# Optimization experiments

Hardware: AMD Instinct MI355X
Metric: run time of the kernel (lower is better)

## Reference

```python
import jax, jax.numpy as jnp
import numpy as np

NUM_TAGS = 5

def setup_inputs() -> dict:
    key = jax.random.key(0)
    ks = jax.random.split(key, 8)
    B, N, K, Q = 2, 5, 5, 4
    Ls, Lq, D = 128, 128, 768
    inp = {
        'support_token_embedding': jax.random.normal(ks[0], (B * N * K, Ls, D), jnp.float32),
        'query_token_embedding': jax.random.normal(ks[1], (B * N * Q, Lq, D), jnp.float32),
        'support_mask': jnp.ones((B * N * K, Ls), jnp.float32),
        'query_mask': jnp.ones((B * N * Q, Lq), jnp.float32),
        'support_entity_label': jax.random.normal(ks[2], (B * N * K, Ls, NUM_TAGS), jnp.float32),
        'proj_w': jax.random.normal(ks[3], (D, 4 * D), jnp.float32) * 0.02,
        'proj_b': jnp.zeros((D,), jnp.float32),
        'rel_w1': jax.random.normal(ks[4], (D, 4 * D), jnp.float32) * 0.02,
        'rel_b1': jnp.zeros((D,), jnp.float32),
        'rel_w2': jax.random.normal(ks[5], (1, D), jnp.float32) * 0.02,
        'rel_b2': jnp.zeros((1,), jnp.float32),
        'B': B, 'N': N, 'K': K, 'Q': Q,
    }
    return inp

def _fuse(m1, m2):
    return jnp.concatenate([m1, m2, jnp.abs(m1 - m2), m1 * m2], axis=-1)

def reference(support_token_embedding, query_token_embedding, support_mask, query_mask,
              support_entity_label, proj_w, proj_b, rel_w1, rel_b1, rel_w2, rel_b2,
              B, N, K, Q):
    D = support_token_embedding.shape[-1]
    Lq = query_token_embedding.shape[1]

    # ---- cal_bio: per-(sample,shot) tag prototypes, vectorized ----
    labels = jnp.argmax(support_entity_label, axis=-1)                 # [BNK, Ls]
    onehot = jax.nn.one_hot(labels, NUM_TAGS, dtype=jnp.float32)       # [BNK, Ls, T]
    # tag 0 ('O') is additionally gated by the support mask
    masks = jnp.concatenate([onehot[:, :, :1] * support_mask[:, :, None], onehot[:, :, 1:]], axis=2)
    sums = jnp.einsum('blt,bld->btd', masks, support_token_embedding)  # [BNK, T, D]
    cnt = jnp.sum(masks, axis=1)[:, :, None]                           # [BNK, T, 1]
    proto = jnp.where(cnt > 0, sums / jnp.maximum(cnt, 1.0), 0.0)      # [BNK, T, D]
    proto = proto.reshape(B * N, K, NUM_TAGS, D).mean(axis=1)          # mean over K shots
    proto = proto.reshape(B, N, NUM_TAGS, D)                           # support_BIO

    # ---- expand to all (query, class) pairs: batch = B*N*Q*N ----
    BQ = B * N * Q * N
    support = jnp.broadcast_to(proto[:, None], (B, N * Q, N, NUM_TAGS, D)).reshape(BQ, NUM_TAGS, D)
    query = jnp.broadcast_to(query_token_embedding.reshape(B, N * Q, 1, Lq, D),
                             (B, N * Q, N, Lq, D)).reshape(BQ, Lq, D)
    qmask = jnp.broadcast_to(query_mask.reshape(B, N * Q, 1, Lq),
                             (B, N * Q, N, Lq)).reshape(BQ, Lq, 1)
    smask = jnp.ones((BQ, NUM_TAGS, 1), jnp.float32)

    # ---- CoAttention with additive mask bias + post-softmax mask multiply ----
    att = jnp.einsum('bsd,bqd->bsq', support, query) + smask * jnp.swapaxes(qmask, 1, 2) * 100.0
    support_ = jnp.einsum('bsq,bqd->bsd', jax.nn.softmax(att, axis=2), query) * smask
    query_ = jnp.einsum('bqs,bsd->bqd', jax.nn.softmax(jnp.swapaxes(att, 1, 2), axis=2), support) * qmask

    # ---- fuse + proj + relu ----
    es = jax.nn.relu(_fuse(support, support_) @ proj_w.T + proj_b)     # [BQ, T, D]
    eq = jax.nn.relu(_fuse(query, query_) @ proj_w.T + proj_b)        # [BQ, Lq, D]

    # ---- local aggregation: masked max + mean pooling ----
    eq_agg = jnp.concatenate([jnp.max(eq, axis=1), jnp.sum(eq, axis=1) / jnp.sum(qmask, axis=1)], axis=1)
    es_agg = jnp.concatenate([jnp.max(es, axis=1), jnp.sum(es, axis=1) / jnp.sum(smask, axis=1)], axis=1)

    # ---- relation MLP ----
    cat_seq = jnp.concatenate([eq_agg, es_agg], axis=1)                # [BQ, 4D]
    h = jax.nn.relu(cat_seq @ rel_w1.T + rel_b1)
    logits = h @ rel_w2.T + rel_b2                                     # [BQ, 1]
    return logits.reshape(B * N * Q, N)
```

## Files before the change

### kernel.cpp

```cpp
#include <hip/hip_runtime.h>

typedef unsigned short u16;
typedef __attribute__((ext_vector_type(8))) short short8;
typedef __attribute__((ext_vector_type(4))) float f32x4;

#define B_   2
#define N_   5
#define K_   5
#define Q_   4
#define T_   5
#define D_   768
#define L_   128
#define BN_  (B_*N_)
#define BNK_ (B_*N_*K_)
#define BQ_  (B_*N_*Q_*N_)
#define K4_  (4*D_)
#define KFQ  1536
#define AROWS 144

#define QEMB_N  (40*128*768)
#define PROJW_N (768*3072)

__device__ __forceinline__ float bf2f(u16 u) {
    return __uint_as_float(((unsigned)u) << 16);
}
__device__ __forceinline__ u16 f2bf(float f) {
    unsigned u = __float_as_uint(f);
    return (u16)((u + 0x7fffu + ((u >> 16) & 1u)) >> 16);
}
__device__ __forceinline__ void gl_lds16(const u16* g, u16* l) {
    __builtin_amdgcn_global_load_lds(
        (const __attribute__((address_space(1))) unsigned int*)g,
        (__attribute__((address_space(3))) unsigned int*)l, 16, 0, 0);
}

__global__ void k_convert3(const float* __restrict__ q, const float* __restrict__ pw,
                           const float* __restrict__ rw, u16* __restrict__ qo,
                           u16* __restrict__ po, u16* __restrict__ ro) {
    const long n1 = QEMB_N / 4, n2 = PROJW_N / 4;
    const long total = n1 + 2 * n2;
    for (long i = (long)blockIdx.x * 256 + threadIdx.x; i < total; i += (long)gridDim.x * 256) {
        const float* src; u16* dst; long k;
        if (i < n1)            { src = q;  dst = qo; k = i; }
        else if (i < n1 + n2)  { src = pw; dst = po; k = i - n1; }
        else                   { src = rw; dst = ro; k = i - n1 - n2; }
        float4 v = ((const float4*)src)[k];
        u16 o[4] = {f2bf(v.x), f2bf(v.y), f2bf(v.z), f2bf(v.w)};
        *(uint2*)(dst + k * 4) = *(const uint2*)o;
    }
}

__global__ void k_proto_shot(const float* __restrict__ label, const float* __restrict__ smask,
                             const float* __restrict__ semb, float* __restrict__ proto_shot) {
    int bnk = blockIdx.x;
    __shared__ int   s_tag[L_];
    __shared__ float s_w[L_];
    __shared__ float s_cnt[T_];
    int tid = threadIdx.x;
    if (tid < L_) {
        const float* lp = label + ((long)bnk * L_ + tid) * T_;
        float best = lp[0]; int bi = 0;
        #pragma unroll
        for (int t = 1; t < T_; ++t) { float v = lp[t]; if (v > best) { best = v; bi = t; } }
        s_tag[tid] = bi;
        s_w[tid]   = (bi == 0) ? smask[(long)bnk * L_ + tid] : 1.0f;
    }
    __syncthreads();
    if (tid < T_) {
        float c = 0.f;
        for (int l = 0; l < L_; ++l) if (s_tag[l] == tid) c += s_w[l];
        s_cnt[tid] = c;
    }
    __syncthreads();
    float acc[3][T_] = {};
    for (int l = 0; l < L_; ++l) {
        float w = s_w[l]; int tg = s_tag[l];
        const float* ep = semb + ((long)bnk * L_ + l) * D_;
        #pragma unroll
        for (int s = 0; s < 3; ++s) {
            float e = ep[tid + s * 256] * w;
            #pragma unroll
            for (int t = 0; t < T_; ++t) acc[s][t] += (tg == t) ? e : 0.0f;
        }
    }
    #pragma unroll
    for (int s = 0; s < 3; ++s) {
        int d = tid + s * 256;
        #pragma unroll
        for (int t = 0; t < T_; ++t) {
            float c = s_cnt[t];
            float v = (c > 0.f) ? acc[s][t] / fmaxf(c, 1.f) : 0.f;
            proto_shot[(bnk * T_ + t) * D_ + d] = v;
        }
    }
}

__global__ void k_proto_mean(const float* __restrict__ proto_shot,
                             float* __restrict__ proto_f32, u16* __restrict__ proto_bf) {
    int idx = blockIdx.x * 256 + threadIdx.x;
    if (idx >= BN_ * T_ * D_) return;
    int bn = idx / (T_ * D_);
    int rem = idx - bn * (T_ * D_);
    float s = 0.f;
    #pragma unroll
    for (int k = 0; k < K_; ++k) s += proto_shot[(bn * K_ + k) * (T_ * D_) + rem];
    s *= (1.f / K_);
    proto_f32[idx] = s;
    proto_bf[idx]  = f2bf(s);
}

__global__ void k_attn(const float* __restrict__ qemb, const float* __restrict__ qmask_g,
                       const float* __restrict__ proto_f32,
                       u16* __restrict__ qf, u16* __restrict__ sup_ws,
                       float* __restrict__ p2m_ws, float* __restrict__ qssum_ws) {
    int x = blockIdx.x;
    int xcd = x & 7, slot = x >> 3;
    int g = (slot / 5) * 8 + xcd;
    int n2 = slot % 5;
    int bq = g * 5 + n2;
    int q_idx = g;
    int bn = (bq / (N_ * Q_ * N_)) * N_ + (bq % N_);
    __shared__ float s_proto[T_ * D_];
    __shared__ float s_att[T_][L_];
    __shared__ float s_ps[T_][L_];
    __shared__ float s_p2[L_][8];
    __shared__ float s_qm[L_];
    int tid = threadIdx.x;
    int w = tid >> 6, lane = tid & 63;
    for (int i = tid; i < T_ * D_; i += 256) s_proto[i] = proto_f32[bn * T_ * D_ + i];
    if (tid < L_) s_qm[tid] = qmask_g[(long)q_idx * L_ + tid];
    __syncthreads();
    for (int p = tid; p < T_ * L_; p += 256) {
        int t = p >> 7, q = p & (L_ - 1);
        const float* pp = s_proto + t * D_;
        const float4* qp = (const float4*)(qemb + ((size_t)q_idx * L_ + q) * D_);
        float acc = 0.f;
        #pragma unroll 4
        for (int d = 0; d < D_ / 4; ++d) {
            float4 v = qp[d];
            acc += v.x * pp[4 * d] + v.y * pp[4 * d + 1] + v.z * pp[4 * d + 2] + v.w * pp[4 * d + 3];
        }
        s_att[t][q] = acc + 100.f * s_qm[q];
    }
    __syncthreads();
    if (tid < T_) {
        int t = tid; float m = -1e30f;
        for (int q = 0; q < L_; ++q) m = fmaxf(m, s_att[t][q]);
        float ss = 0.f;
        for (int q = 0; q < L_; ++q) { float e = __expf(s_att[t][q] - m); s_ps[t][q] = e; ss += e; }
        float inv = 1.f / ss;
        for (int q = 0; q < L_; ++q) s_ps[t][q] *= inv;
    } else if (tid >= 128) {
        int q = tid - 128; float m = -1e30f;
        float e[T_];
        #pragma unroll
        for (int t = 0; t < T_; ++t) m = fmaxf(m, s_att[t][q]);
        float ss = 0.f;
        #pragma unroll
        for (int t = 0; t < T_; ++t) { e[t] = __expf(s_att[t][q] - m); ss += e[t]; }
        float inv = s_qm[q] / ss;
        #pragma unroll
        for (int t = 0; t < T_; ++t) {
            s_p2[q][t] = e[t] * inv;
            p2m_ws[((size_t)bq * T_ + t) * L_ + q] = e[t] * inv;
        }
    } else if (tid == 5) {
        float s = 0.f;
        for (int q = 0; q < L_; ++q) s += s_qm[q];
        qssum_ws[bq] = s;
    }
    __syncthreads();
    u16* qfb = qf + (size_t)bq * AROWS * KFQ;
    {
        float acc[T_][3] = {};
        #pragma unroll 4
        for (int q = 0; q < L_; ++q) {
            const float* qp = qemb + ((size_t)q_idx * L_ + q) * D_;
            float qv[3];
            #pragma unroll
            for (int s = 0; s < 3; ++s) qv[s] = qp[tid + s * 256];
            #pragma unroll
            for (int t = 0; t < T_; ++t) {
                float p = s_ps[t][q];
                #pragma unroll
                for (int s = 0; s < 3; ++s) acc[t][s] += p * qv[s];
            }
        }
        #pragma unroll
        for (int t = 0; t < T_; ++t) {
            u16* er = qfb + (size_t)(128 + t) * KFQ;
            #pragma unroll
            for (int s = 0; s < 3; ++s) {
                int d = tid + s * 256;
                float p = s_proto[t * D_ + d];
                float sv = acc[t][s];
                sup_ws[((size_t)bq * T_ + t) * D_ + d] = f2bf(sv);
                er[d]       = f2bf(fabsf(p - sv));
                er[768 + d] = f2bf(p * sv);
            }
        }
    }
    for (int rr = 0; rr < 32; ++rr) {
        int row = w * 32 + rr;
        float p0 = s_p2[row][0], p1 = s_p2[row][1], p2v = s_p2[row][2];
        float p3 = s_p2[row][3], p4 = s_p2[row][4];
        const float* qrow = qemb + ((size_t)q_idx * L_ + row) * D_;
        u16* qr = qfb + (size_t)row * KFQ;
        #pragma unroll
        for (int pass = 0; pass < 2; ++pass) {
            int u = lane + pass * 64;
            if (u < 96) {
                int d = u * 8;
                float4 a0 = *(const float4*)(qrow + d);
                float4 a1 = *(const float4*)(qrow + d + 4);
                float qv[8] = {a0.x, a0.y, a0.z, a0.w, a1.x, a1.y, a1.z, a1.w};
                short8 o2, o3;
                #pragma unroll
                for (int i = 0; i < 8; ++i) {
                    float m2 = p0 * s_proto[d + i] + p1 * s_proto[D_ + d + i]
                             + p2v * s_proto[2 * D_ + d + i] + p3 * s_proto[3 * D_ + d + i]
                             + p4 * s_proto[4 * D_ + d + i];
                    o2[i] = (short)f2bf(fabsf(qv[i] - m2));
                    o3[i] = (short)f2bf(qv[i] * m2);
                }
                *(short8*)(qr + d)       = o2;
                *(short8*)(qr + 768 + d) = o3;
            }
        }
    }
    {
        u16* pr = qfb + (size_t)133 * KFQ;
        short8 z = short8{0, 0, 0, 0, 0, 0, 0, 0};
        for (int i = tid; i < (11 * KFQ) / 8; i += 256) *(short8*)(pr + i * 8) = z;
    }
}

#define SWZ(g, r) (((g) << 4) + ((r) ^ ((g) << 2)))
__global__ __launch_bounds__(256) void k_gemm_g1(const u16* __restrict__ qemb_bf,
                                                 const u16* __restrict__ proto_bf,
                                                 const u16* __restrict__ projw_bf,
                                                 u16* __restrict__ g1) {
    int mbase = blockIdx.y * 128;
    int jbase = blockIdx.x * 128;
    __shared__ __align__(16) u16 sA[8 * 512];
    __shared__ __align__(16) u16 sB[8 * 512];
    int tid = threadIdx.x;
    int lane = tid & 63, w = tid >> 6, quad = lane >> 4, l16 = lane & 15;
    f32x4 zero = {0.f, 0.f, 0.f, 0.f};
    f32x4 acc[8][2];
    #pragma unroll
    for (int rt = 0; rt < 8; ++rt) { acc[rt][0] = zero; acc[rt][1] = zero; }

    for (int kt = 0; kt < 24; ++kt) {
        int k0 = kt * 32;
        __syncthreads();
        #pragma unroll
        for (int j = 0; j < 2; ++j) {
            int v = tid + j * 256, row = v >> 2, g = v & 3;
            *(uint4*)(sB + (((row >> 4) << 6) + SWZ(g, row & 15)) * 8) =
                *(const uint4*)(projw_bf + (size_t)(jbase + row) * K4_ + k0 + g * 8);
            int grow = mbase + row;
            uint4 av = uint4{0u, 0u, 0u, 0u};
            if (grow < 5120)      av = *(const uint4*)(qemb_bf + (size_t)grow * D_ + k0 + g * 8);
            else if (grow < 5170) av = *(const uint4*)(proto_bf + (size_t)(grow - 5120) * D_ + k0 + g * 8);
            *(uint4*)(sA + (((row >> 4) << 6) + SWZ(g, row & 15)) * 8) = av;
        }
        __syncthreads();
        short8 af[8], bfr[2];
        #pragma unroll
        for (int rt = 0; rt < 8; ++rt)
            af[rt] = *(const short8*)(sA + ((rt << 6) + SWZ(quad, l16)) * 8);
        #pragma unroll
        for (int jj = 0; jj < 2; ++jj)
            bfr[jj] = *(const short8*)(sB + (((w * 2 + jj) << 6) + SWZ(quad, l16)) * 8);
        #pragma unroll
        for (int rt = 0; rt < 8; ++rt)
            #pragma unroll
            for (int jj = 0; jj < 2; ++jj)
                acc[rt][jj] = __builtin_amdgcn_mfma_f32_16x16x32_bf16(af[rt], bfr[jj], acc[rt][jj], 0, 0, 0);
    }
    #pragma unroll
    for (int jj = 0; jj < 2; ++jj) {
        int col = jbase + (w * 2 + jj) * 16 + l16;
        #pragma unroll
        for (int rt = 0; rt < 8; ++rt)
            #pragma unroll
            for (int r = 0; r < 4; ++r) {
                int row = mbase + rt * 16 + quad * 4 + r;
                g1[(size_t)row * D_ + col] = f2bf(acc[rt][jj][r]);
            }
    }
}

__global__ __launch_bounds__(256) void k_gemm_w2(const u16* __restrict__ sup_ws,
                                                 const u16* __restrict__ proto_bf,
                                                 const u16* __restrict__ projw_bf,
                                                 u16* __restrict__ sw2, u16* __restrict__ pw2) {
    int mbase = blockIdx.y * 128;
    int jbase = blockIdx.x * 128;
    __shared__ __align__(16) u16 sA[8 * 512];
    __shared__ __align__(16) u16 sB[8 * 512];
    int tid = threadIdx.x;
    int lane = tid & 63, w = tid >> 6, quad = lane >> 4, l16 = lane & 15;
    f32x4 zero = {0.f, 0.f, 0.f, 0.f};
    f32x4 acc[8][2];
    #pragma unroll
    for (int rt = 0; rt < 8; ++rt) { acc[rt][0] = zero; acc[rt][1] = zero; }

    for (int kt = 0; kt < 24; ++kt) {
        int k0 = kt * 32;
        __syncthreads();
        #pragma unroll
        for (int j = 0; j < 2; ++j) {
            int v = tid + j * 256, row = v >> 2, g = v & 3;
            *(uint4*)(sB + (((row >> 4) << 6) + SWZ(g, row & 15)) * 8) =
                *(const uint4*)(projw_bf + (size_t)(jbase + row) * K4_ + 768 + k0 + g * 8);
            int grow = mbase + row;
            uint4 av = uint4{0u, 0u, 0u, 0u};
            if (grow < 1000)      av = *(const uint4*)(sup_ws + (size_t)grow * D_ + k0 + g * 8);
            else if (grow < 1050) av = *(const uint4*)(proto_bf + (size_t)(grow - 1000) * D_ + k0 + g * 8);
            *(uint4*)(sA + (((row >> 4) << 6) + SWZ(g, row & 15)) * 8) = av;
        }
        __syncthreads();
        short8 af[8], bfr[2];
        #pragma unroll
        for (int rt = 0; rt < 8; ++rt)
            af[rt] = *(const short8*)(sA + ((rt << 6) + SWZ(quad, l16)) * 8);
        #pragma unroll
        for (int jj = 0; jj < 2; ++jj)
            bfr[jj] = *(const short8*)(sB + (((w * 2 + jj) << 6) + SWZ(quad, l16)) * 8);
        #pragma unroll
        for (int rt = 0; rt < 8; ++rt)
            #pragma unroll
            for (int jj = 0; jj < 2; ++jj)
                acc[rt][jj] = __builtin_amdgcn_mfma_f32_16x16x32_bf16(af[rt], bfr[jj], acc[rt][jj], 0, 0, 0);
    }
    #pragma unroll
    for (int jj = 0; jj < 2; ++jj) {
        int col = jbase + (w * 2 + jj) * 16 + l16;
        #pragma unroll
        for (int rt = 0; rt < 8; ++rt)
            #pragma unroll
            for (int r = 0; r < 4; ++r) {
                int row = mbase + rt * 16 + quad * 4 + r;
                if (row < 1000)      sw2[(size_t)row * D_ + col] = f2bf(acc[rt][jj][r]);
                else if (row < 1050) pw2[(size_t)(row - 1000) * D_ + col] = f2bf(acc[rt][jj][r]);
            }
    }
}

__global__ __launch_bounds__(256) void k_gemm_q(
        const u16* __restrict__ qf, const u16* __restrict__ projw_bf,
        const float* __restrict__ projb, const u16* __restrict__ g1,
        const u16* __restrict__ pw2, const u16* __restrict__ sw2,
        const float* __restrict__ p2m, const float* __restrict__ qssum_ws,
        u16* __restrict__ cat_ws) {
    int x = blockIdx.x;
    int xcd = x & 7, slot = x >> 3;
    int bq = (slot / 6) * 8 + xcd;
    int jbase = (slot % 6) * 128;
    int q_idx = bq / N_;
    int bn = (bq / (N_ * Q_ * N_)) * N_ + (bq % N_);
    __shared__ __align__(16) u16 sA[AROWS * 32];
    __shared__ __align__(16) u16 sB[128 * 32];
    __shared__ float s_p2mL[T_ * 128];
    __shared__ float s_pw2L[T_ * 128];
    int tid = threadIdx.x;
    int lane = tid & 63, w = tid >> 6, quad = lane >> 4, l16 = lane & 15;
    int srow = lane >> 2, sko = lane & 3;
    const u16* Ab = qf + (size_t)bq * AROWS * KFQ + (size_t)srow * KFQ + sko * 8;
    const u16* Bb = projw_bf + (size_t)jbase * K4_ + 1536 + (size_t)srow * K4_ + sko * 8;
    u16* lA0 = sA + (w * 16) * 32;
    u16* lA1 = sA + (64 + w * 16) * 32;
    u16* lA2 = sA + 128 * 32;
    u16* lB0 = sB + (w * 16) * 32;
    u16* lB1 = sB + (64 + w * 16) * 32;

    f32x4 zero = {0.f, 0.f, 0.f, 0.f};
    f32x4 acc[9][2];
    #pragma unroll
    for (int rt = 0; rt < 9; ++rt) { acc[rt][0] = zero; acc[rt][1] = zero; }

    for (int kt = 0; kt < KFQ / 32; ++kt) {
        int k0 = kt * 32;
        __syncthreads();
        gl_lds16(Ab + (size_t)(w * 16) * KFQ + k0, lA0);
        gl_lds16(Ab + (size_t)(64 + w * 16) * KFQ + k0, lA1);
        if (w == 0) gl_lds16(Ab + (size_t)128 * KFQ + k0, lA2);
        gl_lds16(Bb + (size_t)(w * 16) * K4_ + k0, lB0);
        gl_lds16(Bb + (size_t)(64 + w * 16) * K4_ + k0, lB1);
        __syncthreads();
        short8 af[9], bfr[2];
        #pragma unroll
        for (int rt = 0; rt < 9; ++rt)
            af[rt] = *(const short8*)(sA + (rt * 16 + l16) * 32 + quad * 8);
        #pragma unroll
        for (int jj = 0; jj < 2; ++jj)
            bfr[jj] = *(const short8*)(sB + ((w * 2 + jj) * 16 + l16) * 32 + quad * 8);
        #pragma unroll
        for (int rt = 0; rt < 9; ++rt)
            #pragma unroll
            for (int jj = 0; jj < 2; ++jj)
                acc[rt][jj] = __builtin_amdgcn_mfma_f32_16x16x32_bf16(af[rt], bfr[jj], acc[rt][jj], 0, 0, 0);
    }
    for (int i = tid; i < T_ * 128; i += 256) {
        s_p2mL[i] = p2m[(size_t)bq * (T_ * 128) + i];
        s_pw2L[i] = bf2f(pw2[(size_t)(bn * T_ + (i >> 7)) * D_ + jbase + (i & 127)]);
    }
    __syncthreads();
    float inv_qs = 1.f / qssum_ws[bq];
    #pragma unroll
    for (int jj = 0; jj < 2; ++jj) {
        int col = jbase + (w * 2 + jj) * 16 + l16;
        int cj = (w * 2 + jj) * 16 + l16;
        float bias = projb[col];
        float qmax = 0.f, qsum = 0.f, smax = 0.f, ssum = 0.f;
        #pragma unroll
        for (int rt = 0; rt < 8; ++rt) {
            #pragma unroll
            for (int r = 0; r < 4; ++r) {
                int row = rt * 16 + quad * 4 + r;
                float g1v = bf2f(g1[(size_t)(q_idx * 128 + row) * D_ + col]);
                float mix = s_p2mL[row] * s_pw2L[cj]
                          + s_p2mL[128 + row] * s_pw2L[128 + cj]
                          + s_p2mL[256 + row] * s_pw2L[256 + cj]
                          + s_p2mL[384 + row] * s_pw2L[384 + cj]
                          + s_p2mL[512 + row] * s_pw2L[512 + cj];
                float v = fmaxf(acc[rt][jj][r] + g1v + mix + bias, 0.f);
                qmax = fmaxf(qmax, v); qsum += v;
            }
        }
        #pragma unroll
        for (int r = 0; r < 4; ++r) {
            int t = quad * 4 + r;
            if (t < T_) {
                float g1v = bf2f(g1[(size_t)(5120 + bn * T_ + t) * D_ + col]);
                float s2v = bf2f(sw2[(size_t)(bq * T_ + t) * D_ + col]);
                float v = fmaxf(acc[8][jj][r] + g1v + s2v + bias, 0.f);
                smax = fmaxf(smax, v); ssum += v;
            }
        }
        qmax = fmaxf(qmax, __shfl_xor(qmax, 16, 64)); qmax = fmaxf(qmax, __shfl_xor(qmax, 32, 64));
        qsum += __shfl_xor(qsum, 16, 64);             qsum += __shfl_xor(qsum, 32, 64);
        smax = fmaxf(smax, __shfl_xor(smax, 16, 64)); smax = fmaxf(smax, __shfl_xor(smax, 32, 64));
        ssum += __shfl_xor(ssum, 16, 64);             ssum += __shfl_xor(ssum, 32, 64);
        if (quad == 0) {
            u16* cp = cat_ws + (size_t)bq * K4_;
            cp[col]           = f2bf(qmax);
            cp[D_ + col]      = f2bf(qsum * inv_qs);
            cp[2 * D_ + col]  = f2bf(smax);
            cp[3 * D_ + col]  = f2bf(ssum * 0.2f);
        }
    }
}

#define AST  40
__global__ __launch_bounds__(256) void k_relmlp(const u16* __restrict__ cat_ws,
                                                const u16* __restrict__ w1,
                                                float* __restrict__ part) {
    int mbase = blockIdx.y * 64;
    int jbase = blockIdx.x * 128;
    int ks = blockIdx.z;
    __shared__ __align__(16) u16 sA[64 * AST];
    __shared__ __align__(16) u16 sB[128 * AST];
    int tid = threadIdx.x;
    int lane = tid & 63, w = tid >> 6, quad = lane >> 4, l16 = lane & 15;
    f32x4 zero = {0.f, 0.f, 0.f, 0.f};
    f32x4 acc[4][2];
    #pragma unroll
    for (int rt = 0; rt < 4; ++rt) { acc[rt][0] = zero; acc[rt][1] = zero; }

    for (int kt = ks * 12; kt < ks * 12 + 12; ++kt) {
        int k0 = kt * 32;
        __syncthreads();
        {
            int row = tid >> 2, ko = (tid & 3) * 8;
            int grow = mbase + row;
            short8 val = short8{0, 0, 0, 0, 0, 0, 0, 0};
            if (grow < BQ_) val = *(const short8*)(cat_ws + (size_t)grow * K4_ + k0 + ko);
            *(short8*)(sA + row * AST + ko) = val;
        }
        for (int u = tid; u < 512; u += 256) {
            int row = u >> 2, ko = (u & 3) * 8;
            *(short8*)(sB + row * AST + ko) =
                *(const short8*)(w1 + (size_t)(jbase + row) * K4_ + k0 + ko);
        }
        __syncthreads();
        short8 af[4], bfr[2];
        #pragma unroll
        for (int rt = 0; rt < 4; ++rt)
            af[rt] = *(const short8*)(sA + (rt * 16 + l16) * AST + quad * 8);
        #pragma unroll
        for (int jj = 0; jj < 2; ++jj)
            bfr[jj] = *(const short8*)(sB + ((2 * w + jj) * 16 + l16) * AST + quad * 8);
        #pragma unroll
        for (int rt = 0; rt < 4; ++rt)
            #pragma unroll
            for (int jj = 0; jj < 2; ++jj)
                acc[rt][jj] = __builtin_amdgcn_mfma_f32_16x16x32_bf16(af[rt], bfr[jj], acc[rt][jj], 0, 0, 0);
    }
    #pragma unroll
    for (int jj = 0; jj < 2; ++jj) {
        int col = jbase + (2 * w + jj) * 16 + l16;
        #pragma unroll
        for (int rt = 0; rt < 4; ++rt) {
            #pragma unroll
            for (int r = 0; r < 4; ++r) {
                int grow = mbase + rt * 16 + quad * 4 + r;
                if (grow < BQ_)
                    part[((size_t)ks * BQ_ + grow) * D_ + col] = acc[rt][jj][r];
            }
        }
    }
}

__global__ void k_rel_fin(const float* __restrict__ part, const float* __restrict__ b1,
                          const float* __restrict__ w2, const float* __restrict__ b2,
                          float* __restrict__ out) {
    int bq = blockIdx.x, tid = threadIdx.x;
    float a = 0.f;
    #pragma unroll
    for (int s = 0; s < 3; ++s) {
        int col = tid + s * 256;
        float sum = 0.f;
        #pragma unroll
        for (int ks = 0; ks < 8; ++ks) sum += part[((size_t)ks * BQ_ + bq) * D_ + col];
        float h = fmaxf(sum + b1[col], 0.f);
        a += h * w2[col];
    }
    __shared__ float red[256];
    red[tid] = a; __syncthreads();
    for (int off = 128; off >= 1; off >>= 1) {
        if (tid < off) red[tid] += red[tid + off];
        __syncthreads();
    }
    if (tid == 0) out[bq] = red[0] + b2[0];
}

extern "C" void kernel_launch(void* const* d_in, const int* in_sizes, int n_in,
                              void* d_out, int out_size, void* d_ws, size_t ws_size,
                              hipStream_t stream) {
    (void)in_sizes; (void)n_in; (void)out_size; (void)ws_size;
    const float* semb  = (const float*)d_in[0];
    const float* qemb  = (const float*)d_in[1];
    const float* smask = (const float*)d_in[2];
    const float* qmask = (const float*)d_in[3];
    const float* label = (const float*)d_in[4];
    const float* projw = (const float*)d_in[5];
    const float* projb = (const float*)d_in[6];
    const float* relw1 = (const float*)d_in[7];
    const float* relb1 = (const float*)d_in[8];
    const float* relw2 = (const float*)d_in[9];
    const float* relb2 = (const float*)d_in[10];

    char* ws = (char*)d_ws;
    u16*   qemb_bf   = (u16*)  (ws + 0);
    u16*   projw_bf  = (u16*)  (ws + 7864320);
    u16*   relw1_bf  = (u16*)  (ws + 12582912);
    float* proto_shot= (float*)(ws + 17301504);
    float* proto_f32 = (float*)(ws + 18069504);
    u16*   proto_bf  = (u16*)  (ws + 18223104);
    float* qssum     = (float*)(ws + 18299904);
    u16*   sup_ws    = (u16*)  (ws + 18300800);
    float* p2m_ws    = (float*)(ws + 19836800);
    u16*   pw2_ws    = (u16*)  (ws + 20348800);
    u16*   sw2_ws    = (u16*)  (ws + 20425600);
    u16*   cat_ws    = (u16*)  (ws + 21961600);
    u16*   g1_ws     = (u16*)  (ws + 23190400);
    float* part_ws   = (float*)(ws + 31251328);
    u16*   qf_ws     = (u16*)  (ws + 36166528);

    k_convert3<<<2048, 256, 0, stream>>>(qemb, projw, relw1, qemb_bf, projw_bf, relw1_bf);
    k_proto_shot<<<BNK_, 256, 0, stream>>>(label, smask, semb, proto_shot);
    k_proto_mean<<<150, 256, 0, stream>>>(proto_shot, proto_f32, proto_bf);
    k_attn<<<BQ_, 256, 0, stream>>>(qemb, qmask, proto_f32, qf_ws, sup_ws, p2m_ws, qssum);
    k_gemm_g1<<<dim3(6, 41), 256, 0, stream>>>(qemb_bf, proto_bf, projw_bf, g1_ws);
    k_gemm_w2<<<dim3(6, 9), 256, 0, stream>>>(sup_ws, proto_bf, projw_bf, sw2_ws, pw2_ws);
    k_gemm_q<<<1200, 256, 0, stream>>>(qf_ws, projw_bf, projb, g1_ws, pw2_ws, sw2_ws,
                                       p2m_ws, qssum, cat_ws);
    k_relmlp<<<dim3(6, 4, 8), 256, 0, stream>>>(cat_ws, relw1_bf, part_ws);
    k_rel_fin<<<BQ_, 256, 0, stream>>>(part_ws, relb1, relw2, relb2, (float*)d_out);
}
```

Baseline: 536.6 us.

## Double-buffer LDS tiles in query projection GEMM to overlap loads with MFMA

Merges the separate A and B shared-memory tiles into one ping-pong buffer pair in k_gemm_q. Each iteration first issues the async global-to-LDS loads for the next k-tile, then runs the MFMAs on the current tile. One barrier per iteration replaces two, so the load latency can hide behind the matrix math. This doubles the kernel's LDS footprint for the tiles, which may reduce how many blocks fit on a CU.

```diff
diff --git a/kernel.cpp b/kernel.cpp
--- a/kernel.cpp
+++ b/kernel.cpp
@@ -361,42 +361,43 @@
     int jbase = (slot % 6) * 128;
     int q_idx = bq / N_;
     int bn = (bq / (N_ * Q_ * N_)) * N_ + (bq % N_);
-    __shared__ __align__(16) u16 sA[AROWS * 32];
-    __shared__ __align__(16) u16 sB[128 * 32];
+    __shared__ __align__(16) u16 sT[2][(AROWS + 128) * 32];
     __shared__ float s_p2mL[T_ * 128];
     __shared__ float s_pw2L[T_ * 128];
     int tid = threadIdx.x;
     int lane = tid & 63, w = tid >> 6, quad = lane >> 4, l16 = lane & 15;
     int srow = lane >> 2, sko = lane & 3;
-    const u16* Ab = qf + (size_t)bq * AROWS * KFQ + (size_t)srow * KFQ + sko * 8;
-    const u16* Bb = projw_bf + (size_t)jbase * K4_ + 1536 + (size_t)srow * K4_ + sko * 8;
-    u16* lA0 = sA + (w * 16) * 32;
-    u16* lA1 = sA + (64 + w * 16) * 32;
-    u16* lA2 = sA + 128 * 32;
-    u16* lB0 = sB + (w * 16) * 32;
-    u16* lB1 = sB + (64 + w * 16) * 32;
+    const u16* Ab = qf + ((size_t)bq * AROWS + srow) * KFQ + sko * 8;
+    const u16* Bb = projw_bf + (size_t)(jbase + srow) * K4_ + 1536 + sko * 8;
 
     f32x4 zero = {0.f, 0.f, 0.f, 0.f};
     f32x4 acc[9][2];
     #pragma unroll
     for (int rt = 0; rt < 9; ++rt) { acc[rt][0] = zero; acc[rt][1] = zero; }
 
+    auto issue = [&](int kt, int b) {
+        int k0 = kt * 32;
+        u16* base = sT[b];
+        gl_lds16(Ab + (size_t)(w * 16) * KFQ + k0, base + (w * 16) * 32);
+        gl_lds16(Ab + (size_t)(64 + w * 16) * KFQ + k0, base + (64 + w * 16) * 32);
+        if (w == 0) gl_lds16(Ab + (size_t)128 * KFQ + k0, base + 128 * 32);
+        gl_lds16(Bb + (size_t)(w * 16) * K4_ + k0, base + (AROWS + w * 16) * 32);
+        gl_lds16(Bb + (size_t)(64 + w * 16) * K4_ + k0, base + (AROWS + 64 + w * 16) * 32);
+    };
+
+    issue(0, 0);
     for (int kt = 0; kt < KFQ / 32; ++kt) {
-        int k0 = kt * 32;
-        __syncthreads();
-        gl_lds16(Ab + (size_t)(w * 16) * KFQ + k0, lA0);
-        gl_lds16(Ab + (size_t)(64 + w * 16) * KFQ + k0, lA1);
-        if (w == 0) gl_lds16(Ab + (size_t)128 * KFQ + k0, lA2);
-        gl_lds16(Bb + (size_t)(w * 16) * K4_ + k0, lB0);
-        gl_lds16(Bb + (size_t)(64 + w * 16) * K4_ + k0, lB1);
-        __syncthreads();
+        int cur = kt & 1;
+        __syncthreads();
+        if (kt + 1 < KFQ / 32) issue(kt + 1, 1 - cur);
+        const u16* base = sT[cur];
         short8 af[9], bfr[2];
         #pragma unroll
         for (int rt = 0; rt < 9; ++rt)
-            af[rt] = *(const short8*)(sA + (rt * 16 + l16) * 32 + quad * 8);
+            af[rt] = *(const short8*)(base + (rt * 16 + l16) * 32 + quad * 8);
         #pragma unroll
         for (int jj = 0; jj < 2; ++jj)
-            bfr[jj] = *(const short8*)(sB + ((w * 2 + jj) * 16 + l16) * 32 + quad * 8);
+            bfr[jj] = *(const short8*)(base + (AROWS + (w * 2 + jj) * 16 + l16) * 32 + quad * 8);
         #pragma unroll
         for (int rt = 0; rt < 9; ++rt)
             #pragma unroll
```

Result: no change. 531.7 us (-0.9%).
